# Optimization experiments

Measured on AMD Instinct MI355X. Metric: run time of the kernel, lower is better.

The kernel has to match this reference:

```python
import jax, jax.numpy as jnp
import numpy as np

B, T, C, H, K = 2, 1024, 2048, 32, 64
D_MIX, D_DEC, FF = 32, 64, 7168
GN_EPS = 1e-5 * 8 ** 2  # GroupNorm eps = 1e-5 * head_size_divisor**2


def setup_inputs() -> dict:
    key = jax.random.key(0)
    ks = jax.random.split(key, 40)
    nrm = lambda i, sh, s=0.02: jax.random.normal(ks[i], sh, jnp.float32) * s
    uni = lambda i, sh: jax.random.uniform(ks[i], sh, jnp.float32)
    return {
        'x': jax.random.normal(ks[0], (B, T, C), jnp.float32),
        'time_mix_shift': jax.random.normal(ks[1], (B, 1, C), jnp.float32),
        'channel_mix_state': jax.random.normal(ks[2], (B, 1, C), jnp.float32),
        'time_mix_state': jax.random.normal(ks[3], (B, H, K, K), jnp.float32) * 0.1,
        'ln1_w': jnp.ones((C,), jnp.float32), 'ln1_b': jnp.zeros((C,), jnp.float32),
        'ln2_w': jnp.ones((C,), jnp.float32), 'ln2_b': jnp.zeros((C,), jnp.float32),
        'maa_x': uni(4, (1, 1, C)), 'maa_w': uni(5, (1, 1, C)), 'maa_k': uni(6, (1, 1, C)),
        'maa_v': uni(7, (1, 1, C)), 'maa_r': uni(8, (1, 1, C)), 'maa_g': uni(9, (1, 1, C)),
        'maa_w1': nrm(10, (C, 5 * D_MIX), 0.01), 'maa_w2': nrm(11, (5, D_MIX, C), 0.01),
        'td': jnp.linspace(-6.0, -1.0, C, dtype=jnp.float32).reshape(1, 1, C),
        'td_w1': nrm(12, (C, D_DEC), 0.01), 'td_w2': nrm(13, (D_DEC, C), 0.01),
        'u': nrm(14, (H, K), 0.05),
        'Wr': nrm(15, (C, C)), 'Wk': nrm(16, (C, C)), 'Wv': nrm(17, (C, C)),
        'Wg': nrm(18, (C, C)), 'Wo': nrm(19, (C, C)),
        'lnx_w': jnp.ones((C,), jnp.float32), 'lnx_b': jnp.zeros((C,), jnp.float32),
        'fmaa_k': uni(20, (1, 1, C)), 'fmaa_r': uni(21, (1, 1, C)),
        'fWk': nrm(22, (FF, C)), 'fWr': nrm(23, (C, C)), 'fWv': nrm(24, (C, FF)),
    }


def _ln(x, w, b, eps=1e-5):
    m = x.mean(-1, keepdims=True)
    v = jnp.var(x, axis=-1, keepdims=True)
    return (x - m) * jax.lax.rsqrt(v + eps) * w + b


def reference(x, time_mix_shift, channel_mix_state, time_mix_state,
              ln1_w, ln1_b, ln2_w, ln2_b,
              maa_x, maa_w, maa_k, maa_v, maa_r, maa_g, maa_w1, maa_w2,
              td, td_w1, td_w2, u, Wr, Wk, Wv, Wg, Wo, lnx_w, lnx_b,
              fmaa_k, fmaa_r, fWk, fWr, fWv):
    # ---- TimeMix (att) on ln1(x) ----
    xn = _ln(x, ln1_w, ln1_b)
    prev = jnp.concatenate([time_mix_shift, xn[:, :-1]], axis=1)  # [B,T,C]
    new_shift = xn[:, -1:]
    xx = prev - xn
    hh = jnp.tanh((xn + xx * maa_x) @ maa_w1).reshape(B, T, 5, D_MIX)
    mm = jnp.einsum('btfd,fdc->fbtc', hh, maa_w2)
    xw = xn + xx * (maa_w + mm[0])
    xk = xn + xx * (maa_k + mm[1])
    xv = xn + xx * (maa_v + mm[2])
    xr = xn + xx * (maa_r + mm[3])
    xg = xn + xx * (maa_g + mm[4])
    r = xr @ Wr.T
    k = xk @ Wk.T
    v = xv @ Wv.T
    g = jax.nn.silu(xg @ Wg.T)
    # log-decay w = -exp(time_decay + LoRA(xw)); per-step decay factor is exp(w)
    w = -jnp.exp(td + jnp.tanh(xw @ td_w1) @ td_w2)
    # WKV6 recurrence over T (state [B,H,K,K])
    rs, ks_, vs, ws = (jnp.moveaxis(a.reshape(B, T, H, K), 1, 0) for a in (r, k, v, w))

    def step(s, inp):
        r_t, k_t, v_t, w_t = inp  # each [B,H,K]
        kv = jnp.einsum('bhk,bhv->bhkv', k_t, v_t)
        o_t = jnp.einsum('bhk,bhkv->bhv', r_t, s + u[None, :, :, None] * kv)
        s = jnp.exp(w_t)[..., None] * s + kv
        return s, o_t

    new_wkv, o = jax.lax.scan(step, time_mix_state, (rs, ks_, vs, ws))
    o = jnp.moveaxis(o, 0, 1)  # [B,T,H,K]
    # GroupNorm over heads (groups=H, channels=K each)
    mu = o.mean(-1, keepdims=True)
    var = jnp.var(o, axis=-1, keepdims=True)
    y = ((o - mu) * jax.lax.rsqrt(var + GN_EPS)).reshape(B, T, C) * lnx_w + lnx_b
    x = x + (y * g) @ Wo.T
    # ---- ChannelMix (ffn) on ln2(x) ----
    xn2 = _ln(x, ln2_w, ln2_b)
    prev2 = jnp.concatenate([channel_mix_state, xn2[:, :-1]], axis=1)
    new_cm = xn2[:, -1:]
    xk2 = prev2 * fmaa_k + xn2 * (1.0 - fmaa_k)
    xr2 = prev2 * fmaa_r + xn2 * (1.0 - fmaa_r)
    kv2 = (jax.nn.relu(xk2 @ fWk.T) ** 2) @ fWv.T
    x = x + jax.nn.sigmoid(xr2 @ fWr.T) * kv2
    return (x, new_shift, new_cm, new_wkv)
```

## Files before the change

kernel.cpp:

```cpp
#include <hip/hip_runtime.h>
#include <hip/hip_bf16.h>
#include <math.h>

#define BB 2
#define TT 1024
#define CC 2048
#define HH 32
#define KK 64
#define BTROWS (BB*TT)
#define FFD 7168
#define LCH 64
#define NCH (TT/LCH)

typedef unsigned short ushort_t;
typedef __bf16 bf16x8 __attribute__((ext_vector_type(8)));
typedef float f32x4 __attribute__((ext_vector_type(4)));

__device__ __forceinline__ ushort_t f2bf(float f) {
  unsigned int u = __float_as_uint(f);
  u += 0x7fff + ((u >> 16) & 1);
  return (ushort_t)(u >> 16);
}

__device__ __forceinline__ void gload16(const ushort_t* g, ushort_t* l) {
  __builtin_amdgcn_global_load_lds(
      (const __attribute__((address_space(1))) void*)g,
      (__attribute__((address_space(3))) void*)l, 16, 0, 0);
}

#define FMA4(a, s, b) { (a).x = fmaf((s), (b).x, (a).x); (a).y = fmaf((s), (b).y, (a).y); \
                        (a).z = fmaf((s), (b).z, (a).z); (a).w = fmaf((s), (b).w, (a).w); }

__global__ __launch_bounds__(256) void cvt_kernel(
    const float* __restrict__ in, ushort_t* __restrict__ out, int n4) {
  int i = blockIdx.x * 256 + threadIdx.x;
  int stride = gridDim.x * 256;
  for (; i < n4; i += stride) {
    float4 v = ((const float4*)in)[i];
    ushort4 o;
    o.x = f2bf(v.x); o.y = f2bf(v.y); o.z = f2bf(v.z); o.w = f2bf(v.w);
    ((ushort4*)out)[i] = o;
  }
}

__global__ __launch_bounds__(256) void ln_kernel(
    const float* __restrict__ x, const float* __restrict__ w,
    const float* __restrict__ b, float* __restrict__ out,
    float* __restrict__ last_out) {
  int row = blockIdx.x;
  const float* xr = x + (size_t)row * CC;
  float vals[8];
  float sum = 0.f, sq = 0.f;
#pragma unroll
  for (int i = 0; i < 8; ++i) {
    float v = xr[threadIdx.x + 256 * i];
    vals[i] = v; sum += v; sq += v * v;
  }
#pragma unroll
  for (int off = 32; off; off >>= 1) {
    sum += __shfl_xor(sum, off);
    sq  += __shfl_xor(sq, off);
  }
  __shared__ float red[2][4];
  int lane = threadIdx.x & 63, wv = threadIdx.x >> 6;
  if (lane == 0) { red[0][wv] = sum; red[1][wv] = sq; }
  __syncthreads();
  sum = red[0][0] + red[0][1] + red[0][2] + red[0][3];
  sq  = red[1][0] + red[1][1] + red[1][2] + red[1][3];
  float mu = sum * (1.f / CC);
  float var = sq * (1.f / CC) - mu * mu;
  float rs = rsqrtf(var + 1e-5f);
  float* orow = out + (size_t)row * CC;
  int t = row % TT;
  float* lrow = (t == TT - 1) ? (last_out + (size_t)(row / TT) * CC) : nullptr;
#pragma unroll
  for (int i = 0; i < 8; ++i) {
    int c = threadIdx.x + 256 * i;
    float y = (vals[i] - mu) * rs * w[c] + b[c];
    orow[c] = y;
    if (lrow) lrow[c] = y;
  }
}

__global__ __launch_bounds__(256) void mixin_kernel(
    const float* __restrict__ xn, const float* __restrict__ tms,
    const float* __restrict__ maa_x, float* __restrict__ out) {
  int idx = blockIdx.x * 256 + threadIdx.x;
  int c = idx & (CC - 1);
  int row = idx >> 11;
  int t = row & (TT - 1);
  int b = row >> 10;
  float xv = xn[idx];
  float pv = (t == 0) ? tms[b * CC + c] : xn[idx - CC];
  out[idx] = xv + (pv - xv) * maa_x[c];
}

__global__ __launch_bounds__(256) void mix2_kernel(
    const float* __restrict__ xn2, const float* __restrict__ cms,
    const float* __restrict__ fk, const float* __restrict__ fr,
    ushort_t* __restrict__ xk2, ushort_t* __restrict__ xr2) {
  int idx = blockIdx.x * 256 + threadIdx.x;
  int c = idx & (CC - 1);
  int row = idx >> 11;
  int t = row & (TT - 1);
  int b = row >> 10;
  float xv = xn2[idx];
  float pv = (t == 0) ? cms[b * CC + c] : xn2[idx - CC];
  float kf = fk[c], rf = fr[c];
  xk2[idx] = f2bf(pv * kf + xv * (1.f - kf));
  xr2[idx] = f2bf(pv * rf + xv * (1.f - rf));
}

__global__ __launch_bounds__(256) void gemm_splitk(
    const float* __restrict__ A, int lda,
    const float* __restrict__ W, int N,
    float* __restrict__ parts, int ntiles, int kslice, int M) {
  __shared__ float As[16][68];
  __shared__ float Ws[16][68];
  const int tid = threadIdx.x;
  const int m0 = blockIdx.x * 64;
  const int n0 = blockIdx.y * 64;
  const int s = blockIdx.z;
  const int kb = s * kslice;
  const int tx = tid & 15, ty = tid >> 4;
  float acc[4][4];
#pragma unroll
  for (int i = 0; i < 4; ++i)
#pragma unroll
    for (int j = 0; j < 4; ++j) acc[i][j] = 0.f;
  for (int k0 = 0; k0 < kslice; k0 += 16) {
    {
      int r = tid >> 2, c = (tid & 3) * 4;
      float4 v = *(const float4*)(A + (size_t)(m0 + r) * lda + kb + k0 + c);
      As[c + 0][r] = v.x; As[c + 1][r] = v.y; As[c + 2][r] = v.z; As[c + 3][r] = v.w;
    }
#pragma unroll
    for (int i = 0; i < 4; ++i) {
      int idx = tid + 256 * i;
      int kr = idx >> 6, nc = idx & 63;
      int n = n0 + nc;
      Ws[kr][nc] = (n < N) ? W[(size_t)(kb + k0 + kr) * N + n] : 0.f;
    }
    __syncthreads();
#pragma unroll
    for (int k = 0; k < 16; ++k) {
      float a[4], w4[4];
#pragma unroll
      for (int i = 0; i < 4; ++i) a[i] = As[k][ty * 4 + i];
#pragma unroll
      for (int j = 0; j < 4; ++j) w4[j] = Ws[k][tx * 4 + j];
#pragma unroll
      for (int i = 0; i < 4; ++i)
#pragma unroll
        for (int j = 0; j < 4; ++j) acc[i][j] = fmaf(a[i], w4[j], acc[i][j]);
    }
    __syncthreads();
  }
  const int NP = ntiles * 64;
  float* pb = parts + (size_t)s * M * NP;
#pragma unroll
  for (int i = 0; i < 4; ++i) {
    int m = m0 + ty * 4 + i;
    float4 v = {acc[i][0], acc[i][1], acc[i][2], acc[i][3]};
    *(float4*)(pb + (size_t)m * NP + n0 + tx * 4) = v;
  }
}

__global__ __launch_bounds__(256) void combine_tanh(
    const float* __restrict__ parts, int NP, int M, int Nreal, int S,
    float* __restrict__ out) {
  int idx = blockIdx.x * 256 + threadIdx.x;
  if (idx >= M * Nreal) return;
  int m = idx / Nreal, n = idx - m * Nreal;
  float acc = 0.f;
  for (int s = 0; s < S; ++s) acc += parts[(size_t)s * M * NP + (size_t)m * NP + n];
  out[idx] = tanhf(acc);
}

__global__ __launch_bounds__(256) void gemm_negexp(
    const float* __restrict__ A, int lda,
    const float* __restrict__ B, int ldb,
    float* __restrict__ out, int N, int K,
    const float* __restrict__ td) {
  __shared__ float As[16][132];
  __shared__ float Bs[16][132];
  const int tid = threadIdx.x;
  const int tx = tid & 15, ty = tid >> 4;
  const int m0 = blockIdx.y * 128, n0 = blockIdx.x * 128;
  float acc[8][8];
#pragma unroll
  for (int i = 0; i < 8; ++i)
#pragma unroll
    for (int j = 0; j < 8; ++j) acc[i][j] = 0.f;
  for (int k0 = 0; k0 < K; k0 += 16) {
    {
      int r = tid >> 1, c = (tid & 1) * 8;
      const float* src = A + (size_t)(m0 + r) * lda + k0 + c;
      float4 v0 = *(const float4*)src;
      float4 v1 = *(const float4*)(src + 4);
      As[c + 0][r] = v0.x; As[c + 1][r] = v0.y; As[c + 2][r] = v0.z; As[c + 3][r] = v0.w;
      As[c + 4][r] = v1.x; As[c + 5][r] = v1.y; As[c + 6][r] = v1.z; As[c + 7][r] = v1.w;
    }
#pragma unroll
    for (int i = 0; i < 2; ++i) {
      int idx = tid + 256 * i;
      int kk = idx >> 5, nn = (idx & 31) * 4;
      float4 v = *(const float4*)(B + (size_t)(k0 + kk) * ldb + n0 + nn);
      *(float4*)&Bs[kk][nn] = v;
    }
    __syncthreads();
#pragma unroll
    for (int k = 0; k < 16; ++k) {
      float a[8], bb[8];
      *(float4*)&a[0] = *(const float4*)&As[k][ty * 8];
      *(float4*)&a[4] = *(const float4*)&As[k][ty * 8 + 4];
      *(float4*)&bb[0] = *(const float4*)&Bs[k][tx * 8];
      *(float4*)&bb[4] = *(const float4*)&Bs[k][tx * 8 + 4];
#pragma unroll
      for (int i = 0; i < 8; ++i)
#pragma unroll
        for (int j = 0; j < 8; ++j) acc[i][j] = fmaf(a[i], bb[j], acc[i][j]);
    }
    __syncthreads();
  }
#pragma unroll
  for (int i = 0; i < 8; ++i) {
    int row = m0 + ty * 8 + i;
#pragma unroll
    for (int j = 0; j < 8; ++j) {
      int col = n0 + tx * 8 + j;
      out[(size_t)row * N + col] = -expf(td[col] + acc[i][j]);
    }
  }
}

struct Mix5Args {
  const float* maa[5];
  float* xw;
  ushort_t* ob[4];
};

__global__ __launch_bounds__(256) void mix5_gemm(
    const float* __restrict__ hh, const float* __restrict__ w2,
    const float* __restrict__ xn, const float* __restrict__ tms, Mix5Args args) {
  const int f = blockIdx.y;
  const int rb = blockIdx.x;
  const int tid = threadIdx.x;
  __shared__ float hh8[8][32];
  {
    int r = tid >> 5, k = tid & 31;
    hh8[r][k] = hh[(size_t)(rb * 8 + r) * 160 + f * 32 + k];
  }
  __syncthreads();
  const float* maa = args.maa[f];
  const float* w2f = w2 + (size_t)f * 32 * CC;
#pragma unroll
  for (int chunk = 0; chunk < 2; ++chunk) {
    const int col = chunk * 1024 + tid * 4;
    float4 w2v[32];
#pragma unroll
    for (int k = 0; k < 32; ++k)
      w2v[k] = *(const float4*)(w2f + (size_t)k * CC + col);
    const float4 maa4 = *(const float4*)(maa + col);
#pragma unroll
    for (int r = 0; r < 8; ++r) {
      const int row = rb * 8 + r;
      float4 acc = {0.f, 0.f, 0.f, 0.f};
#pragma unroll
      for (int k4 = 0; k4 < 8; ++k4) {
        float4 h = *(const float4*)&hh8[r][k4 * 4];
        FMA4(acc, h.x, w2v[k4 * 4 + 0]);
        FMA4(acc, h.y, w2v[k4 * 4 + 1]);
        FMA4(acc, h.z, w2v[k4 * 4 + 2]);
        FMA4(acc, h.w, w2v[k4 * 4 + 3]);
      }
      const int t = row & (TT - 1);
      const size_t oi = (size_t)row * CC + col;
      float4 xv = *(const float4*)(xn + oi);
      float4 pv;
      if (t == 0) pv = *(const float4*)(tms + (size_t)(row >> 10) * CC + col);
      else        pv = *(const float4*)(xn + oi - CC);
      float4 v;
      v.x = xv.x + (pv.x - xv.x) * (maa4.x + acc.x);
      v.y = xv.y + (pv.y - xv.y) * (maa4.y + acc.y);
      v.z = xv.z + (pv.z - xv.z) * (maa4.z + acc.z);
      v.w = xv.w + (pv.w - xv.w) * (maa4.w + acc.w);
      if (f == 0) {
        *(float4*)(args.xw + oi) = v;
      } else {
        ushort4 o;
        o.x = f2bf(v.x); o.y = f2bf(v.y); o.z = f2bf(v.z); o.w = f2bf(v.w);
        *(ushort4*)(args.ob[f - 1] + oi) = o;
      }
    }
  }
}


template <bool IS_A>
__device__ __forceinline__ void g9_stage(
    char* buf, const ushort_t* g, int ld, int r0, int k0, int tid) {
  constexpr int NJ = IS_A ? 4 : 2;
  char* dst = buf + (IS_A ? 0 : 32768);
#pragma unroll
  for (int j = 0; j < NJ; ++j) {
    int L = j * 8192 + tid * 16;
    int P = L ^ (((L >> 7) & 7) << 4);
    int r = P >> 7, cb = (P & 127) >> 1;
    gload16(g + (size_t)(r0 + r) * ld + k0 + cb, (ushort_t*)(dst + L));
  }
}

__device__ __forceinline__ void g9_core(
    const ushort_t* gA, int lda, const ushort_t* gB, int ldb,
    int m0, int n0, int kstart, int K, char* lds, f32x4 (*acc)[4]) {
  const int tid = threadIdx.x, w = tid >> 6, l = tid & 63;
  const int wr = w >> 1, wc = w & 1;
  const int r16 = l & 15, h16 = (l >> 4) * 16;
  const int NT = K >> 6;
  g9_stage<true>(lds, gA, lda, m0, kstart, tid);
  g9_stage<false>(lds, gB, ldb, n0, kstart, tid);
  g9_stage<true>(lds + 49152, gA, lda, m0, kstart + 64, tid);
  g9_stage<false>(lds + 49152, gB, ldb, n0, kstart + 64, tid);
  int cur = 0;
  for (int t = 0; t < NT; ++t) {
    char* bufc = lds + cur * 49152;
    int nxt = cur + 2; if (nxt >= 3) nxt -= 3;
    char* bufn = lds + nxt * 49152;
    if (t + 1 < NT) asm volatile("s_waitcnt vmcnt(6)" ::: "memory");
    else            asm volatile("s_waitcnt vmcnt(0)" ::: "memory");
    __builtin_amdgcn_s_barrier();
    const bool pf = (t + 2 < NT);
    const int k2 = kstart + (t + 2) * 64;
    {
      bf16x8 a[4], b[4];
#pragma unroll
      for (int mf = 0; mf < 4; ++mf) {
        int row = wr * 64 + mf * 16 + r16;
        int off = h16 ^ ((row & 7) << 4);
        a[mf] = *(const bf16x8*)(bufc + row * 128 + off);
      }
#pragma unroll
      for (int nf = 0; nf < 4; ++nf) {
        int row = wc * 64 + nf * 16 + r16;
        int off = h16 ^ ((row & 7) << 4);
        b[nf] = *(const bf16x8*)(bufc + 32768 + row * 128 + off);
      }
      if (pf) g9_stage<true>(bufn, gA, lda, m0, k2, tid);
      __builtin_amdgcn_s_setprio(1);
#pragma unroll
      for (int mf = 0; mf < 4; ++mf)
#pragma unroll
        for (int nf = 0; nf < 4; ++nf)
          acc[mf][nf] = __builtin_amdgcn_mfma_f32_16x16x32_bf16(a[mf], b[nf], acc[mf][nf], 0, 0, 0);
      __builtin_amdgcn_s_setprio(0);
    }
    {
      bf16x8 a[4], b[4];
#pragma unroll
      for (int mf = 0; mf < 4; ++mf) {
        int row = wr * 64 + mf * 16 + r16;
        int off = (64 + h16) ^ ((row & 7) << 4);
        a[mf] = *(const bf16x8*)(bufc + row * 128 + off);
      }
#pragma unroll
      for (int nf = 0; nf < 4; ++nf) {
        int row = wc * 64 + nf * 16 + r16;
        int off = (64 + h16) ^ ((row & 7) << 4);
        b[nf] = *(const bf16x8*)(bufc + 32768 + row * 128 + off);
      }
      if (pf) g9_stage<false>(bufn, gB, ldb, n0, k2, tid);
      __builtin_amdgcn_s_setprio(1);
#pragma unroll
      for (int mf = 0; mf < 4; ++mf)
#pragma unroll
        for (int nf = 0; nf < 4; ++nf)
          acc[mf][nf] = __builtin_amdgcn_mfma_f32_16x16x32_bf16(a[mf], b[nf], acc[mf][nf], 0, 0, 0);
      __builtin_amdgcn_s_setprio(0);
    }
    cur += 1; if (cur == 3) cur = 0;
  }
}

#define G9_INIT_ACC f32x4 acc[4][4]; \
  _Pragma("unroll") for (int i0 = 0; i0 < 4; ++i0) \
  _Pragma("unroll") for (int i1 = 0; i1 < 4; ++i1) acc[i0][i1] = {0.f, 0.f, 0.f, 0.f};

struct RkvgArgs {
  const ushort_t* A[4];
  const ushort_t* W[4];
  float* O[4];
};

__global__ __launch_bounds__(512, 2) void g9_rkvg(RkvgArgs args) {
  __shared__ __align__(16) char lds[147456];
  const int z = blockIdx.z;
  const int m0 = blockIdx.y * 256, n0 = blockIdx.x * 128;
  G9_INIT_ACC
  g9_core(args.A[z], CC, args.W[z], CC, m0, n0, 0, CC, lds, acc);
  const int tid = threadIdx.x, w = tid >> 6, l = tid & 63;
  const int wr = w >> 1, wc = w & 1, r16 = l & 15, q4 = (l >> 4) * 4;
  float* out = args.O[z];
  const bool silu = (z == 3);
#pragma unroll
  for (int mf = 0; mf < 4; ++mf)
#pragma unroll
    for (int nf = 0; nf < 4; ++nf) {
      int col = n0 + wc * 64 + nf * 16 + r16;
#pragma unroll
      for (int j = 0; j < 4; ++j) {
        int row = m0 + wr * 64 + mf * 16 + q4 + j;
        float v = acc[mf][nf][j];
        if (silu) v = v / (1.f + expf(-v));
        out[(size_t)row * CC + col] = v;
      }
    }
}

__global__ __launch_bounds__(512, 2) void g9_relu2(
    const ushort_t* __restrict__ A, int lda,
    const ushort_t* __restrict__ W, int ldb,
    ushort_t* __restrict__ out, int N, int K) {
  __shared__ __align__(16) char lds[147456];
  const int m0 = blockIdx.y * 256, n0 = blockIdx.x * 128;
  G9_INIT_ACC
  g9_core(A, lda, W, ldb, m0, n0, 0, K, lds, acc);
  const int tid = threadIdx.x, w = tid >> 6, l = tid & 63;
  const int wr = w >> 1, wc = w & 1, r16 = l & 15, q4 = (l >> 4) * 4;
#pragma unroll
  for (int mf = 0; mf < 4; ++mf)
#pragma unroll
    for (int nf = 0; nf < 4; ++nf) {
      int col = n0 + wc * 64 + nf * 16 + r16;
#pragma unroll
      for (int j = 0; j < 4; ++j) {
        int row = m0 + wr * 64 + mf * 16 + q4 + j;
        float r_ = fmaxf(acc[mf][nf][j], 0.f);
        out[(size_t)row * N + col] = f2bf(r_ * r_);
      }
    }
}

struct SkArgs {
  const ushort_t* A;
  const ushort_t* W;
  float* P[2];
  int lda, ldb, klen;
};

__global__ __launch_bounds__(512, 2) void g9_sk(SkArgs args) {
  __shared__ __align__(16) char lds[147456];
  const int z = blockIdx.z;
  const int m0 = blockIdx.y * 256, n0 = blockIdx.x * 128;
  G9_INIT_ACC
  g9_core(args.A, args.lda, args.W, args.ldb, m0, n0, z * args.klen, args.klen, lds, acc);
  const int tid = threadIdx.x, w = tid >> 6, l = tid & 63;
  const int wr = w >> 1, wc = w & 1, r16 = l & 15, q4 = (l >> 4) * 4;
  float* out = args.P[z];
#pragma unroll
  for (int mf = 0; mf < 4; ++mf)
#pragma unroll
    for (int nf = 0; nf < 4; ++nf) {
      int col = n0 + wc * 64 + nf * 16 + r16;
#pragma unroll
      for (int j = 0; j < 4; ++j) {
        int row = m0 + wr * 64 + mf * 16 + q4 + j;
        out[(size_t)row * CC + col] = acc[mf][nf][j];
      }
    }
}

__global__ __launch_bounds__(256) void comb_add2(
    const float* __restrict__ p0, const float* __restrict__ p1,
    const float* __restrict__ base, float* __restrict__ out, int n4) {
  int i = blockIdx.x * 256 + threadIdx.x;
  int stride = gridDim.x * 256;
  for (; i < n4; i += stride) {
    float4 a = ((const float4*)p0)[i];
    float4 b = ((const float4*)p1)[i];
    float4 c = ((const float4*)base)[i];
    float4 o = {c.x + a.x + b.x, c.y + a.y + b.y, c.z + a.z + b.z, c.w + a.w + b.w};
    ((float4*)out)[i] = o;
  }
}

__global__ __launch_bounds__(256) void comb_sig2(
    const float* __restrict__ p0, const float* __restrict__ p1,
    float* __restrict__ out, int n4) {
  int i = blockIdx.x * 256 + threadIdx.x;
  int stride = gridDim.x * 256;
  for (; i < n4; i += stride) {
    float4 a = ((const float4*)p0)[i];
    float4 b = ((const float4*)p1)[i];
    float4 o;
    o.x = 1.f / (1.f + expf(-(a.x + b.x)));
    o.y = 1.f / (1.f + expf(-(a.y + b.y)));
    o.z = 1.f / (1.f + expf(-(a.z + b.z)));
    o.w = 1.f / (1.f + expf(-(a.w + b.w)));
    ((float4*)out)[i] = o;
  }
}

__global__ __launch_bounds__(256) void comb_fma2(
    const float* __restrict__ p0, const float* __restrict__ p1,
    const float* __restrict__ x2, const float* __restrict__ sig,
    float* __restrict__ out, int n4) {
  int i = blockIdx.x * 256 + threadIdx.x;
  int stride = gridDim.x * 256;
  for (; i < n4; i += stride) {
    float4 a = ((const float4*)p0)[i];
    float4 b = ((const float4*)p1)[i];
    float4 xx = ((const float4*)x2)[i];
    float4 ss = ((const float4*)sig)[i];
    float4 o;
    o.x = fmaf(ss.x, a.x + b.x, xx.x);
    o.y = fmaf(ss.y, a.y + b.y, xx.y);
    o.z = fmaf(ss.z, a.z + b.z, xx.z);
    o.w = fmaf(ss.w, a.w + b.w, xx.w);
    ((float4*)out)[i] = o;
  }
}

__global__ __launch_bounds__(256) void wkv_chunk1(
    const float* __restrict__ r, const float* __restrict__ k,
    const float* __restrict__ v, const float* __restrict__ w,
    const float* __restrict__ u,
    float* __restrict__ rtG, float* __restrict__ Pg,
    float* __restrict__ dg, float* __restrict__ o_intra) {
  __shared__ __align__(16) float lds[4 * 4160];
  float* Ech = lds;
  float* Ach = lds;
  float* rtl = lds + 4160;
  float* ktl = lds + 2 * 4160;
  float* Vl  = lds + 3 * 4160;
  __shared__ float Dl[64], dl[64];
  const int c = blockIdx.x, bh = blockIdx.y;
  const int b = bh >> 5, h = bh & 31;
  const int tid = threadIdx.x;
  const size_t base = (size_t)b * TT * CC + (size_t)(c * LCH) * CC + h * KK;
  for (int i = 0; i < 16; ++i) {
    int e = tid + 256 * i;
    int row = e >> 6, col = e & 63;
    size_t g = base + (size_t)row * CC + col;
    rtl[row * 65 + col] = r[g];
    ktl[row * 65 + col] = k[g];
    Vl[row * 65 + col] = v[g];
  }
  if (tid < 64) {
    float cum = 0.f;
#pragma unroll 8
    for (int i = 0; i < 64; ++i) {
      cum += w[base + (size_t)i * CC + tid];
      Ech[i * 64 + tid] = cum;
    }
    float dd = expf(cum);
    dl[tid] = dd;
    dg[(size_t)(bh * NCH + c) * 64 + tid] = dd;
  }
  __syncthreads();
  {
    const int g = tid >> 6, kk = tid & 63;
    const float uk = u[h * KK + kk];
    for (int i = 0; i < 16; ++i) {
      int t = i * 4 + g;
      float Cv = Ech[t * 64 + kk];
      float Ev = (t == 0) ? 0.f : Ech[(t - 1) * 64 + kk];
      float rraw = rtl[t * 65 + kk];
      float kraw = ktl[t * 65 + kk];
      float rtv = rraw * expf(Ev);
      float ktv = kraw * expf(-Cv);
      rtl[t * 65 + kk] = rtv;
      ktl[t * 65 + kk] = ktv;
      rtG[((size_t)(bh * NCH + c) * 64 + t) * 64 + kk] = rtv;
      float prod = rraw * uk * kraw;
#pragma unroll
      for (int off = 32; off; off >>= 1) prod += __shfl_xor(prod, off);
      if (kk == 0) Dl[t] = prod;
    }
  }
  __syncthreads();
  {
    const int ti = tid >> 4, tj = tid & 15;
    float a4[4][4];
#pragma unroll
    for (int a = 0; a < 4; ++a)
#pragma unroll
      for (int q = 0; q < 4; ++q) a4[a][q] = 0.f;
    for (int kk = 0; kk < 64; ++kk) {
      float ra[4], kb[4];
#pragma unroll
      for (int a = 0; a < 4; ++a) ra[a] = rtl[(4 * ti + a) * 65 + kk];
#pragma unroll
      for (int q = 0; q < 4; ++q) kb[q] = ktl[(4 * tj + q) * 65 + kk];
#pragma unroll
      for (int a = 0; a < 4; ++a)
#pragma unroll
        for (int q = 0; q < 4; ++q) a4[a][q] = fmaf(ra[a], kb[q], a4[a][q]);
    }
#pragma unroll
    for (int a = 0; a < 4; ++a) {
      int i = 4 * ti + a;
#pragma unroll
      for (int q = 0; q < 4; ++q) {
        int j = 4 * tj + q;
        Ach[i * 65 + j] = (j < i) ? a4[a][q] : (j == i ? Dl[i] : 0.f);
      }
    }
  }
  __syncthreads();
  {
    const int tr = tid >> 4, tv = tid & 15;
    float o4[4][4], p4[4][4];
#pragma unroll
    for (int a = 0; a < 4; ++a)
#pragma unroll
      for (int q = 0; q < 4; ++q) { o4[a][q] = 0.f; p4[a][q] = 0.f; }
    for (int j = 0; j < 64; ++j) {
      float av[4], kv4[4], vv[4];
#pragma unroll
      for (int a = 0; a < 4; ++a) av[a] = Ach[(4 * tr + a) * 65 + j];
#pragma unroll
      for (int a = 0; a < 4; ++a) kv4[a] = ktl[j * 65 + 4 * tr + a];
#pragma unroll
      for (int q = 0; q < 4; ++q) vv[q] = Vl[j * 65 + 4 * tv + q];
#pragma unroll
      for (int a = 0; a < 4; ++a)
#pragma unroll
        for (int q = 0; q < 4; ++q) {
          o4[a][q] = fmaf(av[a], vv[q], o4[a][q]);
          p4[a][q] = fmaf(kv4[a], vv[q], p4[a][q]);
        }
    }
#pragma unroll
    for (int a = 0; a < 4; ++a) {
      int i = 4 * tr + a;
      float4 ov = {o4[a][0], o4[a][1], o4[a][2], o4[a][3]};
      *(float4*)(o_intra + base + (size_t)i * CC + 4 * tv) = ov;
    }
#pragma unroll
    for (int a = 0; a < 4; ++a) {
      int kk2 = 4 * tr + a;
      float dd = dl[kk2];
      float4 pv = {p4[a][0] * dd, p4[a][1] * dd, p4[a][2] * dd, p4[a][3] * dd};
      *(float4*)(Pg + ((size_t)(bh * NCH + c) * 64 + kk2) * 64 + 4 * tv) = pv;
    }
  }
}

__global__ __launch_bounds__(256) void wkv_chain(
    const float* __restrict__ P, const float* __restrict__ d,
    const float* __restrict__ s0, float* __restrict__ s_starts,
    float* __restrict__ s_out) {
  const int bh = blockIdx.x;
  const int tid = threadIdx.x;
  float s[16];
#pragma unroll
  for (int m = 0; m < 16; ++m) s[m] = s0[(size_t)bh * 4096 + tid + 256 * m];
  for (int c = 0; c < NCH; ++c) {
    size_t cb = (size_t)(bh * NCH + c) * 4096;
#pragma unroll
    for (int m = 0; m < 16; ++m) {
      int idx = tid + 256 * m;
      s_starts[cb + idx] = s[m];
      float dd = d[(size_t)(bh * NCH + c) * 64 + (idx >> 6)];
      s[m] = fmaf(dd, s[m], P[cb + idx]);
    }
  }
#pragma unroll
  for (int m = 0; m < 16; ++m) s_out[(size_t)bh * 4096 + tid + 256 * m] = s[m];
}

__global__ __launch_bounds__(256) void wkv_chunk2(
    const float* __restrict__ rtG, const float* __restrict__ s_starts,
    const float* __restrict__ o_intra, const float* __restrict__ g,
    const float* __restrict__ lnw, const float* __restrict__ lnb,
    ushort_t* __restrict__ ym) {
  __shared__ __align__(16) float lds[3 * 4160];
  float* rtl = lds;
  float* sl  = lds + 4160;
  float* ol  = lds + 2 * 4160;
  __shared__ float mul[64], rsl[64];
  const int c = blockIdx.x, bh = blockIdx.y;
  const int b = bh >> 5, h = bh & 31;
  const int tid = threadIdx.x;
  const size_t base = (size_t)b * TT * CC + (size_t)(c * LCH) * CC + h * KK;
  const size_t cb = (size_t)(bh * NCH + c) * 4096;
  for (int i = 0; i < 16; ++i) {
    int e = tid + 256 * i;
    int row = e >> 6, col = e & 63;
    rtl[row * 65 + col] = rtG[cb + e];
    sl[row * 65 + col] = s_starts[cb + e];
  }
  __syncthreads();
  {
    const int tr = tid >> 4, tv = tid & 15;
    float o4[4][4];
#pragma unroll
    for (int a = 0; a < 4; ++a)
#pragma unroll
      for (int q = 0; q < 4; ++q) o4[a][q] = 0.f;
    for (int kk = 0; kk < 64; ++kk) {
      float ra[4], sv[4];
#pragma unroll
      for (int a = 0; a < 4; ++a) ra[a] = rtl[(4 * tr + a) * 65 + kk];
#pragma unroll
      for (int q = 0; q < 4; ++q) sv[q] = sl[kk * 65 + 4 * tv + q];
#pragma unroll
      for (int a = 0; a < 4; ++a)
#pragma unroll
        for (int q = 0; q < 4; ++q) o4[a][q] = fmaf(ra[a], sv[q], o4[a][q]);
    }
#pragma unroll
    for (int a = 0; a < 4; ++a) {
      int i = 4 * tr + a;
      float4 oi = *(const float4*)(o_intra + base + (size_t)i * CC + 4 * tv);
      ol[i * 65 + 4 * tv + 0] = o4[a][0] + oi.x;
      ol[i * 65 + 4 * tv + 1] = o4[a][1] + oi.y;
      ol[i * 65 + 4 * tv + 2] = o4[a][2] + oi.z;
      ol[i * 65 + 4 * tv + 3] = o4[a][3] + oi.w;
    }
  }
  __syncthreads();
  {
    int row = tid >> 2, q = tid & 3;
    float sum = 0.f, sq = 0.f;
#pragma unroll
    for (int j = 0; j < 16; ++j) {
      float val = ol[row * 65 + q * 16 + j];
      sum += val; sq += val * val;
    }
    sum += __shfl_xor(sum, 1); sq += __shfl_xor(sq, 1);
    sum += __shfl_xor(sum, 2); sq += __shfl_xor(sq, 2);
    if (q == 0) {
      float mu = sum * (1.f / 64.f);
      float var = sq * (1.f / 64.f) - mu * mu;
      mul[row] = mu;
      rsl[row] = rsqrtf(var + 6.4e-4f);
    }
  }
  __syncthreads();
  for (int i = 0; i < 16; ++i) {
    int e = tid + 256 * i;
    int row = e >> 6, col = e & 63;
    float val = (ol[row * 65 + col] - mul[row]) * rsl[row];
    val = val * lnw[h * KK + col] + lnb[h * KK + col];
    size_t gi = base + (size_t)row * CC + col;
    ym[gi] = f2bf(val * g[gi]);
  }
}

extern "C" void kernel_launch(void* const* d_in, const int* in_sizes, int n_in,
                              void* d_out, int out_size, void* d_ws, size_t ws_size,
                              hipStream_t stream) {
  const float* x    = (const float*)d_in[0];
  const float* tms  = (const float*)d_in[1];
  const float* cms  = (const float*)d_in[2];
  const float* tmstate = (const float*)d_in[3];
  const float* ln1_w = (const float*)d_in[4];
  const float* ln1_b = (const float*)d_in[5];
  const float* ln2_w = (const float*)d_in[6];
  const float* ln2_b = (const float*)d_in[7];
  const float* maa_x = (const float*)d_in[8];
  const float* maa_w = (const float*)d_in[9];
  const float* maa_k = (const float*)d_in[10];
  const float* maa_v = (const float*)d_in[11];
  const float* maa_r = (const float*)d_in[12];
  const float* maa_g = (const float*)d_in[13];
  const float* maa_w1 = (const float*)d_in[14];
  const float* maa_w2 = (const float*)d_in[15];
  const float* td    = (const float*)d_in[16];
  const float* td_w1 = (const float*)d_in[17];
  const float* td_w2 = (const float*)d_in[18];
  const float* u     = (const float*)d_in[19];
  const float* Wr    = (const float*)d_in[20];
  const float* Wk    = (const float*)d_in[21];
  const float* Wv    = (const float*)d_in[22];
  const float* Wg    = (const float*)d_in[23];
  const float* Wo    = (const float*)d_in[24];
  const float* lnx_w = (const float*)d_in[25];
  const float* lnx_b = (const float*)d_in[26];
  const float* fmk   = (const float*)d_in[27];
  const float* fmr   = (const float*)d_in[28];
  const float* fWk   = (const float*)d_in[29];
  const float* fWr   = (const float*)d_in[30];
  const float* fWv   = (const float*)d_in[31];
  (void)in_sizes; (void)n_in; (void)out_size;

  const size_t SLOT = (size_t)BTROWS * CC;
  float* F[7];
  for (int i = 0; i < 7; ++i) F[i] = (float*)d_ws + i * SLOT;
  ushort_t* B0 = (ushort_t*)((float*)d_ws + 7 * SLOT);
  ushort_t* B1 = B0 + SLOT;
  ushort_t* B2 = B1 + SLOT;
  ushort_t* B3 = B2 + SLOT;
  ushort_t* WBIG = B3 + SLOT;
  ushort_t* WrB = WBIG;
  ushort_t* WkB = WrB + (size_t)CC * CC;
  ushort_t* WvB = WkB + (size_t)CC * CC;
  ushort_t* WgB = WvB + (size_t)CC * CC;
  ushort_t* WoB = WBIG + (size_t)4 * CC * CC;
  ushort_t* fWvB = WoB + (size_t)CC * CC;
  float* hh  = (float*)(fWvB + (size_t)CC * FFD);
  float* tmpd = hh + (size_t)BTROWS * 160;
  size_t need = (size_t)((char*)(tmpd + (size_t)BTROWS * 64) - (char*)d_ws);
  if (ws_size < need) return;
  ushort_t* fWkB = WBIG;
  ushort_t* fWrB = WoB;
  ushort_t* h1   = (ushort_t*)F[5];

  float* rtG = F[1];
  float* o_intra = F[0];
  float* s_starts = (float*)B0;
  float* Pg = (float*)B2;
  float* dbuf = (float*)(WBIG + (size_t)FFD * CC);
  ushort_t* ym = B3;

  float* partsW1 = F[4];
  float* partsTD = F[5];

  float* out_x    = (float*)d_out;
  float* out_shift = out_x + (size_t)BB * TT * CC;
  float* out_cm   = out_shift + (size_t)BB * CC;
  float* out_wkv  = out_cm + (size_t)BB * CC;

  const dim3 blk256(256);
  const dim3 blk512(512);

  cvt_kernel<<<2048, blk256, 0, stream>>>(Wr, WrB, CC * CC / 4);
  cvt_kernel<<<2048, blk256, 0, stream>>>(Wk, WkB, CC * CC / 4);
  cvt_kernel<<<2048, blk256, 0, stream>>>(Wv, WvB, CC * CC / 4);
  cvt_kernel<<<2048, blk256, 0, stream>>>(Wg, WgB, CC * CC / 4);
  cvt_kernel<<<2048, blk256, 0, stream>>>(Wo, WoB, CC * CC / 4);
  cvt_kernel<<<2048, blk256, 0, stream>>>(fWv, fWvB, CC * FFD / 4);

  ln_kernel<<<BTROWS, blk256, 0, stream>>>(x, ln1_w, ln1_b, F[0], out_shift);
  mixin_kernel<<<(BTROWS * CC) / 256, blk256, 0, stream>>>(F[0], tms, maa_x, F[3]);
  gemm_splitk<<<dim3(BTROWS / 64, 3, 8), blk256, 0, stream>>>(
      F[3], CC, maa_w1, 160, partsW1, 3, CC / 8, BTROWS);
  combine_tanh<<<(BTROWS * 160 + 255) / 256, blk256, 0, stream>>>(
      partsW1, 192, BTROWS, 160, 8, hh);
  {
    Mix5Args ma;
    ma.maa[0] = maa_w; ma.maa[1] = maa_k; ma.maa[2] = maa_v; ma.maa[3] = maa_r; ma.maa[4] = maa_g;
    ma.xw = F[1];
    ma.ob[0] = B1; ma.ob[1] = B2; ma.ob[2] = B3; ma.ob[3] = B0;
    mix5_gemm<<<dim3(BTROWS / 8, 5), blk256, 0, stream>>>(hh, maa_w2, F[0], tms, ma);
  }
  gemm_splitk<<<dim3(BTROWS / 64, 1, 8), blk256, 0, stream>>>(
      F[1], CC, td_w1, 64, partsTD, 1, CC / 8, BTROWS);
  combine_tanh<<<(BTROWS * 64 + 255) / 256, blk256, 0, stream>>>(
      partsTD, 64, BTROWS, 64, 8, tmpd);
  gemm_negexp<<<dim3(16, 16), blk256, 0, stream>>>(tmpd, 64, td_w2, CC, F[2], CC, 64, td);
  {
    RkvgArgs ra;
    ra.A[0] = B3; ra.A[1] = B1; ra.A[2] = B2; ra.A[3] = B0;
    ra.W[0] = WrB; ra.W[1] = WkB; ra.W[2] = WvB; ra.W[3] = WgB;
    ra.O[0] = F[3]; ra.O[1] = F[4]; ra.O[2] = F[5]; ra.O[3] = F[6];
    g9_rkvg<<<dim3(16, 8, 4), blk512, 0, stream>>>(ra);
  }
  cvt_kernel<<<2048, blk256, 0, stream>>>(fWk, fWkB, FFD * CC / 4);
  wkv_chunk1<<<dim3(NCH, BB * HH), blk256, 0, stream>>>(
      F[3], F[4], F[5], F[2], u, rtG, Pg, dbuf, o_intra);
  wkv_chain<<<BB * HH, blk256, 0, stream>>>(Pg, dbuf, tmstate, s_starts, out_wkv);
  wkv_chunk2<<<dim3(NCH, BB * HH), blk256, 0, stream>>>(
      rtG, s_starts, o_intra, F[6], lnx_w, lnx_b, ym);
  {
    SkArgs sa;
    sa.A = ym; sa.W = WoB; sa.lda = CC; sa.ldb = CC; sa.klen = CC / 2;
    sa.P[0] = F[0]; sa.P[1] = F[1];
    g9_sk<<<dim3(16, 8, 2), blk512, 0, stream>>>(sa);
  }
  comb_add2<<<2048, blk256, 0, stream>>>(F[0], F[1], x, F[2], (int)(SLOT / 4));
  cvt_kernel<<<2048, blk256, 0, stream>>>(fWr, fWrB, CC * CC / 4);
  ln_kernel<<<BTROWS, blk256, 0, stream>>>(F[2], ln2_w, ln2_b, F[1], out_cm);
  mix2_kernel<<<(BTROWS * CC) / 256, blk256, 0, stream>>>(F[1], cms, fmk, fmr, B1, B2);
  g9_relu2<<<dim3(FFD / 128, 8), blk512, 0, stream>>>(B1, CC, fWkB, CC, h1, FFD, CC);
  {
    SkArgs ss;
    ss.A = B2; ss.W = fWrB; ss.lda = CC; ss.ldb = CC; ss.klen = CC / 2;
    ss.P[0] = F[0]; ss.P[1] = F[1];
    g9_sk<<<dim3(16, 8, 2), blk512, 0, stream>>>(ss);
  }
  comb_sig2<<<2048, blk256, 0, stream>>>(F[0], F[1], F[4], (int)(SLOT / 4));
  {
    SkArgs sf;
    sf.A = h1; sf.W = fWvB; sf.lda = FFD; sf.ldb = FFD; sf.klen = FFD / 2;
    sf.P[0] = F[0]; sf.P[1] = F[3];
    g9_sk<<<dim3(16, 8, 2), blk512, 0, stream>>>(sf);
  }
  comb_fma2<<<2048, blk256, 0, stream>>>(
      F[0], F[3], F[2], F[4], out_x, (int)(SLOT / 4));
}
```

Measured before the change: 679.1 us.

## Store r/k/v/g as bf16, fuse residual add with LN2, batch weight casts

The r/k/v/g projection GEMM now writes bf16 outputs instead of fp32. The WKV chunk kernels read these bf16 values and widen them to fp32, which roughly halves the traffic for four B*T*C tensors. The residual combine and the second LayerNorm are merged into one row kernel, and five separate weight-cast launches become one batched launch. Rounding r/k/v/g to bf16 adds error in the recurrence inputs. The fused LN writes F[1] while also reading it as p1, which is safe only because each thread reads its own elements before writing them.

New measurement: 701.2 us. 1.03x slower.

```diff
diff --git a/kernel.cpp b/kernel.cpp
--- a/kernel.cpp
+++ b/kernel.cpp
@@ -22,6 +22,10 @@
   return (ushort_t)(u >> 16);
 }
 
+__device__ __forceinline__ float b2f(ushort_t b) {
+  return __uint_as_float(((unsigned int)b) << 16);
+}
+
 __device__ __forceinline__ void gload16(const ushort_t* g, ushort_t* l) {
   __builtin_amdgcn_global_load_lds(
       (const __attribute__((address_space(1))) void*)g,
@@ -33,6 +37,26 @@
 
 __global__ __launch_bounds__(256) void cvt_kernel(
     const float* __restrict__ in, ushort_t* __restrict__ out, int n4) {
+  int i = blockIdx.x * 256 + threadIdx.x;
+  int stride = gridDim.x * 256;
+  for (; i < n4; i += stride) {
+    float4 v = ((const float4*)in)[i];
+    ushort4 o;
+    o.x = f2bf(v.x); o.y = f2bf(v.y); o.z = f2bf(v.z); o.w = f2bf(v.w);
+    ((ushort4*)out)[i] = o;
+  }
+}
+
+struct Cvt5Args {
+  const float* in[5];
+  ushort_t* out[5];
+};
+
+__global__ __launch_bounds__(256) void cvt5_kernel(Cvt5Args args) {
+  const int z = blockIdx.y;
+  const float* in = args.in[z];
+  ushort_t* out = args.out[z];
+  const int n4 = CC * CC / 4;
   int i = blockIdx.x * 256 + threadIdx.x;
   int stride = gridDim.x * 256;
   for (; i < n4; i += stride) {
@@ -78,6 +102,48 @@
     int c = threadIdx.x + 256 * i;
     float y = (vals[i] - mu) * rs * w[c] + b[c];
     orow[c] = y;
+    if (lrow) lrow[c] = y;
+  }
+}
+
+__global__ __launch_bounds__(256) void add_ln_kernel(
+    const float* __restrict__ p0, const float* __restrict__ p1,
+    const float* __restrict__ x, const float* __restrict__ w,
+    const float* __restrict__ b, float* __restrict__ x2out,
+    float* __restrict__ xnout, float* __restrict__ last_out) {
+  int row = blockIdx.x;
+  const size_t rb = (size_t)row * CC;
+  float vals[8];
+  float sum = 0.f, sq = 0.f;
+#pragma unroll
+  for (int i = 0; i < 8; ++i) {
+    int c = threadIdx.x + 256 * i;
+    float v = x[rb + c] + p0[rb + c] + p1[rb + c];
+    vals[i] = v; sum += v; sq += v * v;
+  }
+#pragma unroll
+  for (int off = 32; off; off >>= 1) {
+    sum += __shfl_xor(sum, off);
+    sq  += __shfl_xor(sq, off);
+  }
+  __shared__ float red[2][4];
+  int lane = threadIdx.x & 63, wv = threadIdx.x >> 6;
+  if (lane == 0) { red[0][wv] = sum; red[1][wv] = sq; }
+  __syncthreads();
+  sum = red[0][0] + red[0][1] + red[0][2] + red[0][3];
+  sq  = red[1][0] + red[1][1] + red[1][2] + red[1][3];
+  float mu = sum * (1.f / CC);
+  float var = sq * (1.f / CC) - mu * mu;
+  float rs = rsqrtf(var + 1e-5f);
+  int t = row % TT;
+  float* lrow = (t == TT - 1) ? (last_out + (size_t)(row / TT) * CC) : nullptr;
+#pragma unroll
+  for (int i = 0; i < 8; ++i) {
+    int c = threadIdx.x + 256 * i;
+    float v = vals[i];
+    x2out[rb + c] = v;
+    float y = (v - mu) * rs * w[c] + b[c];
+    xnout[rb + c] = y;
     if (lrow) lrow[c] = y;
   }
 }
@@ -296,7 +362,6 @@
   }
 }
 
-
 template <bool IS_A>
 __device__ __forceinline__ void g9_stage(
     char* buf, const ushort_t* g, int ld, int r0, int k0, int tid) {
@@ -389,7 +454,7 @@
 struct RkvgArgs {
   const ushort_t* A[4];
   const ushort_t* W[4];
-  float* O[4];
+  ushort_t* O[4];
 };
 
 __global__ __launch_bounds__(512, 2) void g9_rkvg(RkvgArgs args) {
@@ -400,7 +465,7 @@
   g9_core(args.A[z], CC, args.W[z], CC, m0, n0, 0, CC, lds, acc);
   const int tid = threadIdx.x, w = tid >> 6, l = tid & 63;
   const int wr = w >> 1, wc = w & 1, r16 = l & 15, q4 = (l >> 4) * 4;
-  float* out = args.O[z];
+  ushort_t* out = args.O[z];
   const bool silu = (z == 3);
 #pragma unroll
   for (int mf = 0; mf < 4; ++mf)
@@ -412,7 +477,7 @@
         int row = m0 + wr * 64 + mf * 16 + q4 + j;
         float v = acc[mf][nf][j];
         if (silu) v = v / (1.f + expf(-v));
-        out[(size_t)row * CC + col] = v;
+        out[(size_t)row * CC + col] = f2bf(v);
       }
     }
 }
@@ -468,20 +533,6 @@
         out[(size_t)row * CC + col] = acc[mf][nf][j];
       }
     }
-}
-
-__global__ __launch_bounds__(256) void comb_add2(
-    const float* __restrict__ p0, const float* __restrict__ p1,
-    const float* __restrict__ base, float* __restrict__ out, int n4) {
-  int i = blockIdx.x * 256 + threadIdx.x;
-  int stride = gridDim.x * 256;
-  for (; i < n4; i += stride) {
-    float4 a = ((const float4*)p0)[i];
-    float4 b = ((const float4*)p1)[i];
-    float4 c = ((const float4*)base)[i];
-    float4 o = {c.x + a.x + b.x, c.y + a.y + b.y, c.z + a.z + b.z, c.w + a.w + b.w};
-    ((float4*)out)[i] = o;
-  }
 }
 
 __global__ __launch_bounds__(256) void comb_sig2(
@@ -522,8 +573,8 @@
 }
 
 __global__ __launch_bounds__(256) void wkv_chunk1(
-    const float* __restrict__ r, const float* __restrict__ k,
-    const float* __restrict__ v, const float* __restrict__ w,
+    const ushort_t* __restrict__ r, const ushort_t* __restrict__ k,
+    const ushort_t* __restrict__ v, const float* __restrict__ w,
     const float* __restrict__ u,
     float* __restrict__ rtG, float* __restrict__ Pg,
     float* __restrict__ dg, float* __restrict__ o_intra) {
@@ -542,9 +593,9 @@
     int e = tid + 256 * i;
     int row = e >> 6, col = e & 63;
     size_t g = base + (size_t)row * CC + col;
-    rtl[row * 65 + col] = r[g];
-    ktl[row * 65 + col] = k[g];
-    Vl[row * 65 + col] = v[g];
+    rtl[row * 65 + col] = b2f(r[g]);
+    ktl[row * 65 + col] = b2f(k[g]);
+    Vl[row * 65 + col] = b2f(v[g]);
   }
   if (tid < 64) {
     float cum = 0.f;
@@ -672,7 +723,7 @@
 
 __global__ __launch_bounds__(256) void wkv_chunk2(
     const float* __restrict__ rtG, const float* __restrict__ s_starts,
-    const float* __restrict__ o_intra, const float* __restrict__ g,
+    const float* __restrict__ o_intra, const ushort_t* __restrict__ g,
     const float* __restrict__ lnw, const float* __restrict__ lnb,
     ushort_t* __restrict__ ym) {
   __shared__ __align__(16) float lds[3 * 4160];
@@ -745,7 +796,7 @@
     float val = (ol[row * 65 + col] - mul[row]) * rsl[row];
     val = val * lnw[h * KK + col] + lnb[h * KK + col];
     size_t gi = base + (size_t)row * CC + col;
-    ym[gi] = f2bf(val * g[gi]);
+    ym[gi] = f2bf(val * b2f(g[gi]));
   }
 }
 
@@ -808,6 +859,11 @@
   ushort_t* fWrB = WoB;
   ushort_t* h1   = (ushort_t*)F[5];
 
+  ushort_t* rB = (ushort_t*)F[3];
+  ushort_t* kB = (ushort_t*)F[4];
+  ushort_t* vB = (ushort_t*)F[5];
+  ushort_t* gB = (ushort_t*)F[6];
+
   float* rtG = F[1];
   float* o_intra = F[0];
   float* s_starts = (float*)B0;
@@ -826,11 +882,12 @@
   const dim3 blk256(256);
   const dim3 blk512(512);
 
-  cvt_kernel<<<2048, blk256, 0, stream>>>(Wr, WrB, CC * CC / 4);
-  cvt_kernel<<<2048, blk256, 0, stream>>>(Wk, WkB, CC * CC / 4);
-  cvt_kernel<<<2048, blk256, 0, stream>>>(Wv, WvB, CC * CC / 4);
-  cvt_kernel<<<2048, blk256, 0, stream>>>(Wg, WgB, CC * CC / 4);
-  cvt_kernel<<<2048, blk256, 0, stream>>>(Wo, WoB, CC * CC / 4);
+  {
+    Cvt5Args ca;
+    ca.in[0] = Wr; ca.in[1] = Wk; ca.in[2] = Wv; ca.in[3] = Wg; ca.in[4] = Wo;
+    ca.out[0] = WrB; ca.out[1] = WkB; ca.out[2] = WvB; ca.out[3] = WgB; ca.out[4] = WoB;
+    cvt5_kernel<<<dim3(512, 5), blk256, 0, stream>>>(ca);
+  }
   cvt_kernel<<<2048, blk256, 0, stream>>>(fWv, fWvB, CC * FFD / 4);
 
   ln_kernel<<<BTROWS, blk256, 0, stream>>>(x, ln1_w, ln1_b, F[0], out_shift);
@@ -855,24 +912,24 @@
     RkvgArgs ra;
     ra.A[0] = B3; ra.A[1] = B1; ra.A[2] = B2; ra.A[3] = B0;
     ra.W[0] = WrB; ra.W[1] = WkB; ra.W[2] = WvB; ra.W[3] = WgB;
-    ra.O[0] = F[3]; ra.O[1] = F[4]; ra.O[2] = F[5]; ra.O[3] = F[6];
+    ra.O[0] = rB; ra.O[1] = kB; ra.O[2] = vB; ra.O[3] = gB;
     g9_rkvg<<<dim3(16, 8, 4), blk512, 0, stream>>>(ra);
   }
   cvt_kernel<<<2048, blk256, 0, stream>>>(fWk, fWkB, FFD * CC / 4);
   wkv_chunk1<<<dim3(NCH, BB * HH), blk256, 0, stream>>>(
-      F[3], F[4], F[5], F[2], u, rtG, Pg, dbuf, o_intra);
+      rB, kB, vB, F[2], u, rtG, Pg, dbuf, o_intra);
   wkv_chain<<<BB * HH, blk256, 0, stream>>>(Pg, dbuf, tmstate, s_starts, out_wkv);
   wkv_chunk2<<<dim3(NCH, BB * HH), blk256, 0, stream>>>(
-      rtG, s_starts, o_intra, F[6], lnx_w, lnx_b, ym);
+      rtG, s_starts, o_intra, gB, lnx_w, lnx_b, ym);
   {
     SkArgs sa;
     sa.A = ym; sa.W = WoB; sa.lda = CC; sa.ldb = CC; sa.klen = CC / 2;
     sa.P[0] = F[0]; sa.P[1] = F[1];
     g9_sk<<<dim3(16, 8, 2), blk512, 0, stream>>>(sa);
   }
-  comb_add2<<<2048, blk256, 0, stream>>>(F[0], F[1], x, F[2], (int)(SLOT / 4));
+  add_ln_kernel<<<BTROWS, blk256, 0, stream>>>(
+      F[0], F[1], x, ln2_w, ln2_b, F[2], F[1], out_cm);
   cvt_kernel<<<2048, blk256, 0, stream>>>(fWr, fWrB, CC * CC / 4);
-  ln_kernel<<<BTROWS, blk256, 0, stream>>>(F[2], ln2_w, ln2_b, F[1], out_cm);
   mix2_kernel<<<(BTROWS * CC) / 256, blk256, 0, stream>>>(F[1], cms, fmk, fmr, B1, B2);
   g9_relu2<<<dim3(FFD / 128, 8), blk512, 0, stream>>>(B1, CC, fWkB, CC, h1, FFD, CC);
   {
```
